# Kernel tuning notes

Measured on AMD Instinct MI355X. Metric: run time of the kernel, lower is better.

Reference implementation:

```python
import jax, jax.numpy as jnp
import numpy as np

MARGIN = 1.0
EPS = 1e-12  # safe sqrt/normalize clamp; used entries have magnitude >> EPS


def _normalize(x):
    return x / jnp.maximum(jnp.linalg.norm(x, axis=-1, keepdims=True), EPS)


def _cdist(x, y):
    # Pairwise L2 distances, matches torch.cdist(p=2)
    sq = (jnp.sum(x * x, axis=-1)[:, None]
          + jnp.sum(y * y, axis=-1)[None, :]
          - 2.0 * (x @ y.T))
    return jnp.sqrt(jnp.maximum(sq, EPS))


def setup_inputs() -> dict:
    key = jax.random.key(0)
    k1, k2, k3 = jax.random.split(key, 3)
    B, P, D = 4096, 2, 256
    anchor = jax.random.normal(k1, (B, D), dtype=jnp.float32)
    positive = jax.random.normal(k2, (B, P, D), dtype=jnp.float32)
    labels = jax.random.randint(k3, (B,), 0, 200)
    return {"anchor": anchor, "positive": positive, "labels": labels}


def reference(anchor, positive, labels):
    a = _normalize(anchor)            # [B, D]
    p = _normalize(positive)          # [B, P, D]
    B = a.shape[0]
    all_labels = jnp.concatenate([labels, labels])           # [2B]
    neg_mask = all_labels[None, :] != labels[:, None]        # [B, 2B]
    idx = jnp.arange(B)
    losses = []
    for v in range(p.shape[1]):  # loop over small fixed num_positives
        feats = jnp.concatenate([a, p[:, v]], axis=0)        # [2B, D]
        dist = _cdist(feats, feats)                          # [2B, 2B]
        pos_dist = dist[idx, idx + B]                        # [B]
        # hard negative mining: min distance over different-label columns
        neg_dist = jnp.min(jnp.where(neg_mask, dist[:B], jnp.inf), axis=1)  # [B]
        losses.append(jnp.maximum(pos_dist - neg_dist + MARGIN, 0.0))
    return jnp.mean(jnp.stack(losses))
```

## Files before the change

kernel.cpp:

```cpp
#include <hip/hip_runtime.h>
#include <hip/hip_bf16.h>

#define NB    4096
#define ND    256
#define NP    2
#define TOT   (NB * 3)
#define NCHUNK 48
#define COLS_PER_CHUNK 256
#define TILES 16
#define IMIN_SENT (-1073741824)
#define INV_SCALE (1.0f / 16129.0f)

typedef float f32x4 __attribute__((ext_vector_type(4)));
typedef int   i32x4 __attribute__((ext_vector_type(4)));

#define WS_F_OFF    0
#define WS_POS_OFF  (TOT * 256)
#define WS_NEG_OFF  (WS_POS_OFF + NB * NP * 4)

__global__ void norm_pos_kernel(const float* __restrict__ anchor,
                                const float* __restrict__ positive,
                                unsigned char* __restrict__ F2,
                                float* __restrict__ posArr,
                                int* __restrict__ negmax) {
    if (blockIdx.x < 48) negmax[blockIdx.x * 256 + threadIdx.x] = IMIN_SENT;

    int wid = threadIdx.x >> 6, lane = threadIdx.x & 63;
    int row = blockIdx.x * 4 + wid;
    int group = row >> 4, r15 = row & 15;
    int kk = lane >> 4, quad = (lane >> 2) & 3, jj = (lane & 3) * 4;
    int* dst = (int*)(F2 + (size_t)group * 4096 + kk * 1024 + (quad * 16 + r15) * 16 + jj);

    if (row < NB) {
        const float* src = anchor + (size_t)row * ND;
        float4 x = *(const float4*)(src + lane * 4);
        float ss = x.x * x.x + x.y * x.y + x.z * x.z + x.w * x.w;
        #pragma unroll
        for (int m = 1; m < 64; m <<= 1) ss += __shfl_xor(ss, m, 64);
        float inv = 127.0f / fmaxf(sqrtf(ss), 1e-12f);
        int b0 = (int)rintf(x.x * inv) & 0xff;
        int b1 = (int)rintf(x.y * inv) & 0xff;
        int b2 = (int)rintf(x.z * inv) & 0xff;
        int b3 = (int)rintf(x.w * inv) & 0xff;
        *dst = b0 | (b1 << 8) | (b2 << 16) | (b3 << 24);
    } else {
        int q = row - NB;
        int v = q >> 12;
        int j = q & (NB - 1);
        const float* sp = positive + (size_t)(j * NP + v) * ND;
        const float* sa = anchor + (size_t)j * ND;
        float4 xp = *(const float4*)(sp + lane * 4);
        float4 xa = *(const float4*)(sa + lane * 4);
        float sspv = xp.x * xp.x + xp.y * xp.y + xp.z * xp.z + xp.w * xp.w;
        float ssa  = xa.x * xa.x + xa.y * xa.y + xa.z * xa.z + xa.w * xa.w;
        float dot  = xa.x * xp.x + xa.y * xp.y + xa.z * xp.z + xa.w * xp.w;
        #pragma unroll
        for (int m = 1; m < 64; m <<= 1) {
            sspv += __shfl_xor(sspv, m, 64);
            ssa  += __shfl_xor(ssa, m, 64);
            dot  += __shfl_xor(dot, m, 64);
        }
        float invp = 127.0f / fmaxf(sqrtf(sspv), 1e-12f);
        int b0 = (int)rintf(xp.x * invp) & 0xff;
        int b1 = (int)rintf(xp.y * invp) & 0xff;
        int b2 = (int)rintf(xp.z * invp) & 0xff;
        int b3 = (int)rintf(xp.w * invp) & 0xff;
        *dst = b0 | (b1 << 8) | (b2 << 16) | (b3 << 24);
        if (lane == 0) {
            float inva = 1.0f / fmaxf(sqrtf(ssa), 1e-12f);
            float invpf = invp * (1.0f / 127.0f);
            float dn = dot * inva * invpf;
            float sq = 2.0f - 2.0f * dn;
            posArr[j * NP + v] = sqrtf(fmaxf(sq, 1e-12f));
        }
    }
}

__global__ __launch_bounds__(512) void gram_max_kernel(
        const unsigned char* __restrict__ F2,
        const int* __restrict__ labels,
        int* __restrict__ negmax) {
    __shared__ int slab[COLS_PER_CHUNK];
    int tid = threadIdx.x;
    int wid = tid >> 6, lane = tid & 63;
    int l15 = lane & 15, quad = lane >> 4;

    int id = blockIdx.x;
    int chunk = id >> 4;
    int rbi   = id & 15;

    int rowBase = rbi * 256 + wid * 32;
    int col0 = chunk * COLS_PER_CHUNK;
    int part = chunk >> 4;

    i32x4 af[2][4];
    #pragma unroll
    for (int s = 0; s < 2; ++s) {
        const unsigned char* ab = F2 + (size_t)(rbi * 16 + wid * 2 + s) * 4096 + lane * 16;
        #pragma unroll
        for (int kk = 0; kk < 4; ++kk)
            af[s][kk] = *(const i32x4*)(ab + kk * 1024);
    }
    unsigned rlp[2];
    #pragma unroll
    for (int s = 0; s < 2; ++s) {
        const int* lb = labels + rowBase + s * 16 + quad * 4;
        rlp[s] = (unsigned)lb[0] | ((unsigned)lb[1] << 8)
               | ((unsigned)lb[2] << 16) | ((unsigned)lb[3] << 24);
    }
    if (tid < COLS_PER_CHUNK) slab[tid] = labels[(col0 & (NB - 1)) + tid];

    int vmax[2][4];
    #pragma unroll
    for (int s = 0; s < 2; ++s)
        #pragma unroll
        for (int r = 0; r < 4; ++r) vmax[s][r] = IMIN_SENT;

    __syncthreads();

    const unsigned char* bbase = F2 + (size_t)chunk * 65536 + lane * 16;
    #pragma unroll 2
    for (int ct = 0; ct < TILES; ++ct) {
        i32x4 bfr[4];
        #pragma unroll
        for (int kk = 0; kk < 4; ++kk)
            bfr[kk] = *(const i32x4*)(bbase + ct * 4096 + kk * 1024);

        int lc = slab[ct * 16 + l15];
        unsigned lcq = (unsigned)lc * 0x01010101u;

        i32x4 acc[2];
        #pragma unroll
        for (int s = 0; s < 2; ++s) acc[s] = (i32x4){0, 0, 0, 0};
        #pragma unroll
        for (int kk = 0; kk < 4; ++kk)
            #pragma unroll
            for (int s = 0; s < 2; ++s)
                acc[s] = __builtin_amdgcn_mfma_i32_16x16x64_i8(af[s][kk], bfr[kk], acc[s], 0, 0, 0);

        #pragma unroll
        for (int s = 0; s < 2; ++s) {
            unsigned x = rlp[s] ^ lcq;
            #pragma unroll
            for (int r = 0; r < 4; ++r) {
                bool neq = ((x >> (8 * r)) & 0xffu) != 0u;
                int cand = neq ? acc[s][r] : IMIN_SENT;
                vmax[s][r] = vmax[s][r] > cand ? vmax[s][r] : cand;
            }
        }
    }

    #pragma unroll
    for (int m = 1; m < 16; m <<= 1)
        #pragma unroll
        for (int s = 0; s < 2; ++s)
            #pragma unroll
            for (int r = 0; r < 4; ++r) {
                int o = __shfl_xor(vmax[s][r], m, 64);
                vmax[s][r] = vmax[s][r] > o ? vmax[s][r] : o;
            }

    if (l15 == 0) {
        #pragma unroll
        for (int s = 0; s < 2; ++s)
            #pragma unroll
            for (int r = 0; r < 4; ++r) {
                int row = rowBase + s * 16 + quad * 4 + r;
                atomicMax(&negmax[part * NB + row], vmax[s][r]);
            }
    }
}

__global__ void finalize_kernel(const int* __restrict__ negmax,
                                const float* __restrict__ posArr,
                                float* __restrict__ out) {
    int row = blockIdx.x * 256 + threadIdx.x;
    int ia = negmax[row];
    int i0 = negmax[NB + row];
    int i1 = negmax[2 * NB + row];
    int m0 = ia > i0 ? ia : i0;
    int m1 = ia > i1 ? ia : i1;
    float d0 = (float)m0 * INV_SCALE;
    float d1 = (float)m1 * INV_SCALE;
    float n0 = sqrtf(fmaxf(2.0f - 2.0f * d0, 1e-12f));
    float n1 = sqrtf(fmaxf(2.0f - 2.0f * d1, 1e-12f));
    float l = fmaxf(posArr[row * 2 + 0] - n0 + 1.0f, 0.0f)
            + fmaxf(posArr[row * 2 + 1] - n1 + 1.0f, 0.0f);
    int lane = threadIdx.x & 63, wid = threadIdx.x >> 6;
    #pragma unroll
    for (int m = 1; m < 64; m <<= 1) l += __shfl_xor(l, m, 64);
    __shared__ float wsum[4];
    if (lane == 0) wsum[wid] = l;
    __syncthreads();
    if (threadIdx.x == 0) {
        float s = wsum[0] + wsum[1] + wsum[2] + wsum[3];
        atomicAdd(out, s * (1.0f / (NB * NP)));
    }
}

extern "C" void kernel_launch(void* const* d_in, const int* in_sizes, int n_in,
                              void* d_out, int out_size, void* d_ws, size_t ws_size,
                              hipStream_t stream) {
    const float* anchor   = (const float*)d_in[0];
    const float* positive = (const float*)d_in[1];
    const int*   labels   = (const int*)d_in[2];
    float* out = (float*)d_out;

    unsigned char* F2 = (unsigned char*)((char*)d_ws + WS_F_OFF);
    float* posArr     = (float*)((char*)d_ws + WS_POS_OFF);
    int*   negmax     = (int*)((char*)d_ws + WS_NEG_OFF);

    hipMemsetAsync(d_out, 0, sizeof(float), stream);
    norm_pos_kernel<<<TOT / 4, 256, 0, stream>>>(anchor, positive, F2, posArr, negmax);
    gram_max_kernel<<<(NB / 256) * NCHUNK, 512, 0, stream>>>(F2, labels, negmax);
    finalize_kernel<<<NB / 256, 256, 0, stream>>>(negmax, posArr, out);
}
```

Measured before the change: 90.26 us.

## Double-buffer B tiles in gram kernel and fold finalize into single block

The gram kernel now prefetches the next column tile's int8 fragments into a second register buffer while MFMAs run on the current one, and raises wave priority around the MFMA burst. The finalize kernel becomes a single 512-thread block that writes the mean directly, which drops the memset launch and the atomicAdd. This targets global-load latency in the inner loop and per-launch overhead, at the cost of more registers for the extra buffer and a serial single-block finalize.

```diff
diff --git a/kernel.cpp b/kernel.cpp
--- a/kernel.cpp
+++ b/kernel.cpp
@@ -76,6 +76,33 @@
     }
 }
 
+__device__ __forceinline__ void mfma_fold(const i32x4 af[2][4],
+                                          const i32x4 buf[4],
+                                          int lc, unsigned rlp0, unsigned rlp1,
+                                          int vmax[2][4]) {
+    unsigned lcq = (unsigned)lc * 0x01010101u;
+    i32x4 acc0 = (i32x4){0, 0, 0, 0};
+    i32x4 acc1 = (i32x4){0, 0, 0, 0};
+    __builtin_amdgcn_s_setprio(1);
+    #pragma unroll
+    for (int kk = 0; kk < 4; ++kk) {
+        acc0 = __builtin_amdgcn_mfma_i32_16x16x64_i8(af[0][kk], buf[kk], acc0, 0, 0, 0);
+        acc1 = __builtin_amdgcn_mfma_i32_16x16x64_i8(af[1][kk], buf[kk], acc1, 0, 0, 0);
+    }
+    __builtin_amdgcn_s_setprio(0);
+    unsigned x0 = rlp0 ^ lcq;
+    unsigned x1 = rlp1 ^ lcq;
+    #pragma unroll
+    for (int r = 0; r < 4; ++r) {
+        bool nq0 = ((x0 >> (8 * r)) & 0xffu) != 0u;
+        bool nq1 = ((x1 >> (8 * r)) & 0xffu) != 0u;
+        int c0 = nq0 ? acc0[r] : IMIN_SENT;
+        int c1 = nq1 ? acc1[r] : IMIN_SENT;
+        vmax[0][r] = vmax[0][r] > c0 ? vmax[0][r] : c0;
+        vmax[1][r] = vmax[1][r] > c1 ? vmax[1][r] : c1;
+    }
+}
+
 __global__ __launch_bounds__(512) void gram_max_kernel(
         const unsigned char* __restrict__ F2,
         const int* __restrict__ labels,
@@ -116,38 +143,27 @@
         #pragma unroll
         for (int r = 0; r < 4; ++r) vmax[s][r] = IMIN_SENT;
 
+    const unsigned char* bbase = F2 + (size_t)chunk * 65536 + lane * 16;
+
+    i32x4 bA[4], bB[4];
+    #pragma unroll
+    for (int kk = 0; kk < 4; ++kk)
+        bA[kk] = *(const i32x4*)(bbase + kk * 1024);
+
     __syncthreads();
 
-    const unsigned char* bbase = F2 + (size_t)chunk * 65536 + lane * 16;
-    #pragma unroll 2
-    for (int ct = 0; ct < TILES; ++ct) {
-        i32x4 bfr[4];
+    #pragma unroll
+    for (int ct = 0; ct < TILES; ct += 2) {
         #pragma unroll
         for (int kk = 0; kk < 4; ++kk)
-            bfr[kk] = *(const i32x4*)(bbase + ct * 4096 + kk * 1024);
-
-        int lc = slab[ct * 16 + l15];
-        unsigned lcq = (unsigned)lc * 0x01010101u;
-
-        i32x4 acc[2];
-        #pragma unroll
-        for (int s = 0; s < 2; ++s) acc[s] = (i32x4){0, 0, 0, 0};
-        #pragma unroll
-        for (int kk = 0; kk < 4; ++kk)
+            bB[kk] = *(const i32x4*)(bbase + (ct + 1) * 4096 + kk * 1024);
+        mfma_fold(af, bA, slab[ct * 16 + l15], rlp[0], rlp[1], vmax);
+        if (ct + 2 < TILES) {
             #pragma unroll
-            for (int s = 0; s < 2; ++s)
-                acc[s] = __builtin_amdgcn_mfma_i32_16x16x64_i8(af[s][kk], bfr[kk], acc[s], 0, 0, 0);
-
-        #pragma unroll
-        for (int s = 0; s < 2; ++s) {
-            unsigned x = rlp[s] ^ lcq;
-            #pragma unroll
-            for (int r = 0; r < 4; ++r) {
-                bool neq = ((x >> (8 * r)) & 0xffu) != 0u;
-                int cand = neq ? acc[s][r] : IMIN_SENT;
-                vmax[s][r] = vmax[s][r] > cand ? vmax[s][r] : cand;
-            }
+            for (int kk = 0; kk < 4; ++kk)
+                bA[kk] = *(const i32x4*)(bbase + (ct + 2) * 4096 + kk * 1024);
         }
+        mfma_fold(af, bB, slab[(ct + 1) * 16 + l15], rlp[0], rlp[1], vmax);
     }
 
     #pragma unroll
@@ -171,30 +187,38 @@
     }
 }
 
-__global__ void finalize_kernel(const int* __restrict__ negmax,
-                                const float* __restrict__ posArr,
-                                float* __restrict__ out) {
-    int row = blockIdx.x * 256 + threadIdx.x;
-    int ia = negmax[row];
-    int i0 = negmax[NB + row];
-    int i1 = negmax[2 * NB + row];
-    int m0 = ia > i0 ? ia : i0;
-    int m1 = ia > i1 ? ia : i1;
-    float d0 = (float)m0 * INV_SCALE;
-    float d1 = (float)m1 * INV_SCALE;
-    float n0 = sqrtf(fmaxf(2.0f - 2.0f * d0, 1e-12f));
-    float n1 = sqrtf(fmaxf(2.0f - 2.0f * d1, 1e-12f));
-    float l = fmaxf(posArr[row * 2 + 0] - n0 + 1.0f, 0.0f)
-            + fmaxf(posArr[row * 2 + 1] - n1 + 1.0f, 0.0f);
-    int lane = threadIdx.x & 63, wid = threadIdx.x >> 6;
-    #pragma unroll
-    for (int m = 1; m < 64; m <<= 1) l += __shfl_xor(l, m, 64);
-    __shared__ float wsum[4];
-    if (lane == 0) wsum[wid] = l;
+__global__ __launch_bounds__(512) void finalize_kernel(
+        const int* __restrict__ negmax,
+        const float* __restrict__ posArr,
+        float* __restrict__ out) {
+    int tid = threadIdx.x;
+    float lsum = 0.0f;
+    #pragma unroll
+    for (int k = 0; k < 8; ++k) {
+        int row = tid + k * 512;
+        int ia = negmax[row];
+        int i0 = negmax[NB + row];
+        int i1 = negmax[2 * NB + row];
+        int m0 = ia > i0 ? ia : i0;
+        int m1 = ia > i1 ? ia : i1;
+        float d0 = (float)m0 * INV_SCALE;
+        float d1 = (float)m1 * INV_SCALE;
+        float n0 = sqrtf(fmaxf(2.0f - 2.0f * d0, 1e-12f));
+        float n1 = sqrtf(fmaxf(2.0f - 2.0f * d1, 1e-12f));
+        float2 pr = *(const float2*)&posArr[row * 2];
+        lsum += fmaxf(pr.x - n0 + 1.0f, 0.0f) + fmaxf(pr.y - n1 + 1.0f, 0.0f);
+    }
+    int lane = tid & 63, wid = tid >> 6;
+    #pragma unroll
+    for (int m = 1; m < 64; m <<= 1) lsum += __shfl_xor(lsum, m, 64);
+    __shared__ float wsum[8];
+    if (lane == 0) wsum[wid] = lsum;
     __syncthreads();
-    if (threadIdx.x == 0) {
-        float s = wsum[0] + wsum[1] + wsum[2] + wsum[3];
-        atomicAdd(out, s * (1.0f / (NB * NP)));
+    if (tid == 0) {
+        float s = 0.0f;
+        #pragma unroll
+        for (int w = 0; w < 8; ++w) s += wsum[w];
+        out[0] = s * (1.0f / (NB * NP));
     }
 }
 
@@ -210,8 +234,7 @@
     float* posArr     = (float*)((char*)d_ws + WS_POS_OFF);
     int*   negmax     = (int*)((char*)d_ws + WS_NEG_OFF);
 
-    hipMemsetAsync(d_out, 0, sizeof(float), stream);
     norm_pos_kernel<<<TOT / 4, 256, 0, stream>>>(anchor, positive, F2, posArr, negmax);
     gram_max_kernel<<<(NB / 256) * NCHUNK, 512, 0, stream>>>(F2, labels, negmax);
-    finalize_kernel<<<NB / 256, 256, 0, stream>>>(negmax, posArr, out);
-}
+    finalize_kernel<<<1, 512, 0, stream>>>(negmax, posArr, out);
+}
```

Measured after the change: 88.04 us. 2.5% less time.
